# Kernel tuning notes

Measured on AMD Instinct MI355X. Metric: run time of the kernel, lower is better.

The kernel has to match this reference:

```python
import jax, jax.numpy as jnp
import numpy as np

N = 50000
E = 800000
IN_C, HID_C, OUT_C = 128, 128, 64


def setup_inputs() -> dict:
    key = jax.random.key(0)
    ks = jax.random.split(key, 12)
    x = jax.random.normal(ks[0], (N, IN_C), dtype=jnp.float32)
    edge_index = jax.random.randint(ks[1], (2, E), 0, N, dtype=jnp.int64)
    dims = [(IN_C, HID_C), (HID_C, HID_C), (HID_C, OUT_C)]
    params = {}
    for i, (din, dout) in enumerate(dims):
        s = 1.0 / np.sqrt(din)
        params[f"Wl{i}"] = jax.random.uniform(ks[2 + 3 * i], (din, dout), jnp.float32, -s, s)
        params[f"b{i}"] = jnp.zeros((dout,), jnp.float32)
        params[f"Wr{i}"] = jax.random.uniform(ks[3 + 3 * i], (din, dout), jnp.float32, -s, s)
    return {"x": x, "edge_index": edge_index, **params}


def _sage_conv(x, src, dst, Wl, b, Wr):
    # mean-aggregate neighbor features: messages flow src -> dst
    agg = jax.ops.segment_sum(x[src], dst, num_segments=N)          # [N, d]
    deg = jax.ops.segment_sum(jnp.ones((src.shape[0],), x.dtype), dst, num_segments=N)
    agg = agg / jnp.maximum(deg, 1.0)[:, None]                      # mean (0 for isolated nodes)
    return agg @ Wl + b + x @ Wr


def reference(x, edge_index, Wl0, b0, Wr0, Wl1, b1, Wr1, Wl2, b2, Wr2):
    src, dst = edge_index[0], edge_index[1]
    h = _sage_conv(x, src, dst, Wl0, b0, Wr0)
    h = jax.nn.relu(h)  # dropout is identity in eval mode
    h = _sage_conv(h, src, dst, Wl1, b1, Wr1)
    h = jax.nn.relu(h)
    h = _sage_conv(h, src, dst, Wl2, b2, Wr2)
    return h
```

## Files before the change

kernel.cpp:

```cpp
#include <hip/hip_runtime.h>

#define N_NODES 50000
#define N_EDGES 800000
#define NBUCK 196
#define NHIST 196

typedef __attribute__((ext_vector_type(8))) short short8;
typedef __attribute__((ext_vector_type(4))) float f32x4;
typedef __attribute__((ext_vector_type(8))) unsigned short ushort8v;
typedef __attribute__((ext_vector_type(16))) unsigned char uchar16;


__device__ inline void split_bf16(float f, unsigned short& hi, unsigned short& lo) {
    union { float f; unsigned u; } a; a.f = f;
    unsigned r = (a.u + 0x7fffu + ((a.u >> 16) & 1u)) >> 16;
    hi = (unsigned short)r;
    union { unsigned u; float f; } b; b.u = r << 16;
    union { float f; unsigned u; } c; c.f = f - b.f;
    unsigned r2 = (c.u + 0x7fffu + ((c.u >> 16) & 1u)) >> 16;
    lo = (unsigned short)r2;
}

__device__ inline unsigned short f2bf(float f) {
    union { float f; unsigned u; } a; a.f = f;
    return (unsigned short)((a.u + 0x7fffu + ((a.u >> 16) & 1u)) >> 16);
}

__device__ inline float bf2f(unsigned short u) {
    union { unsigned u; float f; } a; a.u = (unsigned)u << 16; return a.f;
}

__device__ inline unsigned char q8(float v, float qs) {
    int qi = (int)rintf(v * qs);
    qi = qi > 127 ? 127 : (qi < -127 ? -127 : qi);
    return (unsigned char)(qi + 128);
}

__device__ inline void acc8(float* a, uint2 w, float s) {
#pragma unroll
    for (int j = 0; j < 4; ++j) {
        a[j]     += (float)((w.x >> (8 * j)) & 255u) * s;
        a[j + 4] += (float)((w.y >> (8 * j)) & 255u) * s;
    }
}


__global__ void prep_kernel(const float* __restrict__ W0, const float* __restrict__ W1,
                            const float* __restrict__ W2, const float* __restrict__ W3,
                            const float* __restrict__ W4, const float* __restrict__ W5,
                            unsigned short* __restrict__ wout,
                            const float* __restrict__ x, unsigned short* __restrict__ xhi,
                            unsigned short* __restrict__ xlo,
                            unsigned char* __restrict__ xq, float* __restrict__ xsc,
                            const int* __restrict__ dst, int* __restrict__ blkhist) {
    __shared__ int lhist[NBUCK];
    if (blockIdx.x < 320) {
        int t = blockIdx.x * 256 + threadIdx.x;
        const float* W; int D, local, half; size_t base;
        if (t < 65536) {
            int mat = t >> 14; local = t & 16383; D = 128; half = 16384;
            base = (size_t)mat * 32768;
            W = mat == 0 ? W0 : mat == 1 ? W1 : mat == 2 ? W2 : W3;
        } else {
            int m = (t - 65536) >> 13; local = (t - 65536) & 8191; D = 64; half = 8192;
            base = 131072 + (size_t)m * 16384;
            W = m == 0 ? W4 : W5;
        }
        int j = local & 7, lane = (local >> 3) & 63, ks = (local >> 9) & 3, ct = local >> 11;
        int k = ks * 32 + ((lane >> 4) << 3) + j;
        int n = (ct << 4) + (lane & 15);
        unsigned short hi, lo;
        split_bf16(W[k * D + n], hi, lo);
        wout[base + local] = hi;
        wout[base + half + local] = lo;
    } else if (blockIdx.x < 1883) {
        int t = (blockIdx.x - 320) * 256 + threadIdx.x;
        if (t >= N_NODES * 8) return;
        const float* p = x + (size_t)t * 16;
        float4 v0 = *(const float4*)(p);
        float4 v1 = *(const float4*)(p + 4);
        float4 v2 = *(const float4*)(p + 8);
        float4 v3 = *(const float4*)(p + 12);
        float vv[16] = {v0.x, v0.y, v0.z, v0.w, v1.x, v1.y, v1.z, v1.w,
                        v2.x, v2.y, v2.z, v2.w, v3.x, v3.y, v3.z, v3.w};
        float m = 0.f;
#pragma unroll
        for (int j = 0; j < 16; ++j) m = fmaxf(m, fabsf(vv[j]));
        m = fmaxf(m, __shfl_xor(m, 1));
        m = fmaxf(m, __shfl_xor(m, 2));
        m = fmaxf(m, __shfl_xor(m, 4));
        float qs = m > 0.f ? 127.0f / m : 0.0f;
        uchar16 qv;
        ushort8v h0, l0, h1, l1;
#pragma unroll
        for (int j = 0; j < 16; ++j) {
            unsigned short a, b;
            split_bf16(vv[j], a, b);
            if (j < 8) { h0[j] = a; l0[j] = b; } else { h1[j - 8] = a; l1[j - 8] = b; }
            qv[j] = q8(vv[j], qs);
        }
        *(ushort8v*)(xhi + (size_t)t * 16) = h0;
        *(ushort8v*)(xhi + (size_t)t * 16 + 8) = h1;
        *(ushort8v*)(xlo + (size_t)t * 16) = l0;
        *(ushort8v*)(xlo + (size_t)t * 16 + 8) = l1;
        *(uchar16*)(xq + (size_t)t * 16) = qv;
        if ((t & 7) == 0) xsc[t >> 3] = m * (1.0f / 127.0f);
    } else {
        const int hb = blockIdx.x - 1883;
        const int base = hb * 4096;
        if (threadIdx.x < NBUCK) lhist[threadIdx.x] = 0;
        __syncthreads();
#pragma unroll
        for (int i = 0; i < 16; ++i) {
            int e = base + i * 256 + threadIdx.x;
            if (e < N_EDGES) atomicAdd(&lhist[dst[e] >> 8], 1);
        }
        __syncthreads();
        if (threadIdx.x < NBUCK) blkhist[hb * NBUCK + threadIdx.x] = lhist[threadIdx.x];
    }
}


__global__ void scan_sums_kernel(const int* __restrict__ blkhist,
                                 int* __restrict__ bucketBase, int* __restrict__ bucketCur,
                                 int* __restrict__ rowptr) {
    __shared__ int s[256];
    int tid = threadIdx.x;
    int v = 0;
    if (tid < NBUCK)
        for (int h = 0; h < NHIST; ++h) v += blkhist[h * NBUCK + tid];
    s[tid] = v;
    __syncthreads();
    for (int off = 1; off < 256; off <<= 1) {
        int t = (tid >= off) ? s[tid - off] : 0;
        __syncthreads();
        s[tid] += t;
        __syncthreads();
    }
    if (tid < NBUCK) {
        int b = s[tid] - v;
        bucketBase[tid] = b;
        bucketCur[tid] = b;
    }
    if (tid == 0) { bucketBase[NBUCK] = N_EDGES; rowptr[N_NODES] = N_EDGES; }
}


__global__ __launch_bounds__(256) void partition_kernel(
    const int* __restrict__ src, const int* __restrict__ dst,
    int* __restrict__ bucketCur, unsigned int* __restrict__ ebuf, int E) {
    __shared__ int hist[NBUCK], binoff[NBUCK], bincur[NBUCK], runstart[NBUCK];
    __shared__ int scanbuf[256];
    __shared__ unsigned int sortbuf[2048];
    const int tid = threadIdx.x;
    const int base = blockIdx.x * 2048;
    if (tid < NBUCK) hist[tid] = 0;
    __syncthreads();
    int myb[8]; unsigned int myp[8];
#pragma unroll
    for (int i = 0; i < 8; ++i) {
        int e = base + i * 256 + tid;
        if (e < E) {
            int d = dst[e], s = src[e];
            myb[i] = d >> 8;
            myp[i] = ((unsigned)d << 16) | (unsigned)s;
            atomicAdd(&hist[myb[i]], 1);
        } else myb[i] = -1;
    }
    __syncthreads();
    int v = (tid < NBUCK) ? hist[tid] : 0;
    scanbuf[tid] = v;
    __syncthreads();
    for (int off = 1; off < 256; off <<= 1) {
        int t = (tid >= off) ? scanbuf[tid - off] : 0;
        __syncthreads();
        scanbuf[tid] += t;
        __syncthreads();
    }
    if (tid < NBUCK) {
        binoff[tid] = scanbuf[tid] - v;
        bincur[tid] = 0;
        runstart[tid] = atomicAdd(&bucketCur[tid], v);
    }
    __syncthreads();
#pragma unroll
    for (int i = 0; i < 8; ++i) {
        if (myb[i] >= 0) {
            int r = atomicAdd(&bincur[myb[i]], 1);
            sortbuf[binoff[myb[i]] + r] = myp[i];
        }
    }
    __syncthreads();
    int nloc = E - base; if (nloc > 2048) nloc = 2048;
#pragma unroll
    for (int i = 0; i < 8; ++i) {
        int idx = i * 256 + tid;
        if (idx < nloc) {
            unsigned int p = sortbuf[idx];
            int b = p >> 24;
            ebuf[runstart[b] + (idx - binoff[b])] = p;
        }
    }
}


__global__ __launch_bounds__(256) void fine_fill_kernel(
    const unsigned int* __restrict__ ebuf, const int* __restrict__ bucketBase,
    int* __restrict__ rowptr, unsigned short* __restrict__ esrc, int n) {
    __shared__ int cnt[256], scanbuf[256], cur[256];
    const int b = blockIdx.x, tid = threadIdx.x;
    const int nbase = b << 8;
    cnt[tid] = 0;
    __syncthreads();
    const int lo = bucketBase[b], hi = bucketBase[b + 1];
    for (int k = lo + tid; k < hi; k += 256)
        atomicAdd(&cnt[(ebuf[k] >> 16) & 255], 1);
    __syncthreads();
    int v = cnt[tid];
    scanbuf[tid] = v;
    __syncthreads();
    for (int off = 1; off < 256; off <<= 1) {
        int t = (tid >= off) ? scanbuf[tid - off] : 0;
        __syncthreads();
        scanbuf[tid] += t;
        __syncthreads();
    }
    int start = lo + scanbuf[tid] - v;
    if (nbase + tid < n) rowptr[nbase + tid] = start;
    cur[tid] = start;
    __syncthreads();
    for (int k = lo + tid; k < hi; k += 256) {
        unsigned int p = ebuf[k];
        int pos = atomicAdd(&cur[(p >> 16) & 255], 1);
        esrc[pos] = (unsigned short)(p & 0xFFFFu);
    }
}


__global__ __launch_bounds__(256, 8) void agg_kernel(
    const unsigned char* __restrict__ Hq, const float* __restrict__ Hsc,
    const int* __restrict__ rowptr, const unsigned short* __restrict__ esrc,
    unsigned short* __restrict__ Ahi, int n) {
    int g = (blockIdx.x * blockDim.x + threadIdx.x) >> 4;
    int l16 = threadIdx.x & 15;
    if (g >= n) return;
    int beg = rowptr[g], end = rowptr[g + 1];
    const unsigned char* __restrict__ Hb = Hq + l16 * 8;
    float a0[8] = {0,0,0,0,0,0,0,0}, a1[8] = {0,0,0,0,0,0,0,0};
    float sacc = 0.f;
    int k = beg;
    for (; k + 6 <= end; k += 6) {
        int e0 = esrc[k],     e1 = esrc[k + 1], e2 = esrc[k + 2];
        int e3 = esrc[k + 3], e4 = esrc[k + 4], e5 = esrc[k + 5];
        uint2 w0 = *(const uint2*)(Hb + (size_t)e0 * 128);
        uint2 w1 = *(const uint2*)(Hb + (size_t)e1 * 128);
        uint2 w2 = *(const uint2*)(Hb + (size_t)e2 * 128);
        uint2 w3 = *(const uint2*)(Hb + (size_t)e3 * 128);
        uint2 w4 = *(const uint2*)(Hb + (size_t)e4 * 128);
        uint2 w5 = *(const uint2*)(Hb + (size_t)e5 * 128);
        float s0 = Hsc[e0], s1 = Hsc[e1], s2 = Hsc[e2];
        float s3 = Hsc[e3], s4 = Hsc[e4], s5 = Hsc[e5];
        acc8(a0, w0, s0); acc8(a1, w1, s1); acc8(a0, w2, s2);
        acc8(a1, w3, s3); acc8(a0, w4, s4); acc8(a1, w5, s5);
        sacc += s0 + s1 + s2 + s3 + s4 + s5;
    }
    for (; k + 2 <= end; k += 2) {
        int e0 = esrc[k], e1 = esrc[k + 1];
        uint2 w0 = *(const uint2*)(Hb + (size_t)e0 * 128);
        uint2 w1 = *(const uint2*)(Hb + (size_t)e1 * 128);
        float s0 = Hsc[e0], s1 = Hsc[e1];
        acc8(a0, w0, s0); acc8(a1, w1, s1);
        sacc += s0 + s1;
    }
    if (k < end) {
        int e0 = esrc[k];
        uint2 w0 = *(const uint2*)(Hb + (size_t)e0 * 128);
        float s0 = Hsc[e0];
        acc8(a0, w0, s0);
        sacc += s0;
    }
    float inv = (end > beg) ? 1.0f / (float)(end - beg) : 0.0f;
    ushort8v mh;
#pragma unroll
    for (int j = 0; j < 8; ++j)
        mh[j] = f2bf((a0[j] + a1[j] - 128.0f * sacc) * inv);
    *(ushort8v*)(Ahi + (size_t)g * 128 + l16 * 8) = mh;
}


template <int DOUT, bool RELU, bool SPLIT_OUT>
__global__ __launch_bounds__(256, 4) void gemm_planes(
    const unsigned short* __restrict__ A1hi,
    const unsigned short* __restrict__ A2hi, const unsigned short* __restrict__ A2lo,
    const unsigned short* __restrict__ B1p, const unsigned short* __restrict__ B2p,
    const float* __restrict__ bias, float* __restrict__ outf,
    unsigned short* __restrict__ outhi, unsigned short* __restrict__ outlo,
    unsigned char* __restrict__ outq, float* __restrict__ outsc, int M) {
    constexpr int K = 128, BM = 32, KS = 4, CT = DOUT / 16, CPW = CT / 4;
    constexpr int PITCH = K + 8;
    constexpr int HALF = CT * KS * 512;
    __shared__ unsigned short As[3][BM * PITCH];
    __shared__ float wmax[BM][4];

    const int tid = threadIdx.x;
    const int r0 = blockIdx.x * BM;

    const unsigned short* __restrict__ srcs[3] = {A1hi, A2hi, A2lo};
#pragma unroll
    for (int s = 0; s < 3; ++s) {
#pragma unroll
        for (int c = 0; c < 2; ++c) {
            int chunk = tid + c * 256;
            int row = chunk >> 4;
            int c8 = (chunk & 15) * 8;
            int grow = r0 + row; if (grow >= M) grow = M - 1;
            *(ushort8v*)(&As[s][row * PITCH + c8]) =
                *(const ushort8v*)(srcs[s] + (size_t)grow * K + c8);
        }
    }
    __syncthreads();

    const int wave = tid >> 6, lane = tid & 63;
    const int rl = lane & 15, quad = lane >> 4;

    f32x4 acc[2][CPW];
#pragma unroll
    for (int c = 0; c < CPW; ++c) {
        float bv = bias[(wave * CPW + c) * 16 + rl];
        acc[0][c] = (f32x4){bv, bv, bv, bv};
        acc[1][c] = acc[0][c];
    }

#pragma unroll
    for (int ks = 0; ks < KS; ++ks) {
        short8 a_ag[2], a_sh[2][2];
#pragma unroll
        for (int rt = 0; rt < 2; ++rt) {
            int off = (rt * 16 + rl) * PITCH + ks * 32 + quad * 8;
            a_ag[rt]    = *(const short8*)(&As[0][off]);
            a_sh[rt][0] = *(const short8*)(&As[1][off]);
            a_sh[rt][1] = *(const short8*)(&As[2][off]);
        }
        short8 b1[CPW][2], b2[CPW][2];
#pragma unroll
        for (int c = 0; c < CPW; ++c) {
            size_t boff = (((wave * CPW + c) * KS + ks) * 64 + lane) * 8;
#pragma unroll
            for (int p = 0; p < 2; ++p) {
                b1[c][p] = *(const short8*)(B1p + p * HALF + boff);
                b2[c][p] = *(const short8*)(B2p + p * HALF + boff);
            }
        }
#pragma unroll
        for (int rt = 0; rt < 2; ++rt)
#pragma unroll
            for (int c = 0; c < CPW; ++c) {
                acc[rt][c] = __builtin_amdgcn_mfma_f32_16x16x32_bf16(a_ag[rt],    b1[c][0], acc[rt][c], 0, 0, 0);
                acc[rt][c] = __builtin_amdgcn_mfma_f32_16x16x32_bf16(a_ag[rt],    b1[c][1], acc[rt][c], 0, 0, 0);
                acc[rt][c] = __builtin_amdgcn_mfma_f32_16x16x32_bf16(a_sh[rt][0], b2[c][0], acc[rt][c], 0, 0, 0);
                acc[rt][c] = __builtin_amdgcn_mfma_f32_16x16x32_bf16(a_sh[rt][0], b2[c][1], acc[rt][c], 0, 0, 0);
                acc[rt][c] = __builtin_amdgcn_mfma_f32_16x16x32_bf16(a_sh[rt][1], b2[c][0], acc[rt][c], 0, 0, 0);
            }
    }

    if (RELU) {
#pragma unroll
        for (int rt = 0; rt < 2; ++rt)
#pragma unroll
            for (int c = 0; c < CPW; ++c)
#pragma unroll
                for (int r = 0; r < 4; ++r)
                    acc[rt][c][r] = fmaxf(acc[rt][c][r], 0.f);
    }

    float qsc[2][4];
    if constexpr (SPLIT_OUT) {
        float lm[2][4];
#pragma unroll
        for (int rt = 0; rt < 2; ++rt)
#pragma unroll
            for (int r = 0; r < 4; ++r) {
                float m = fabsf(acc[rt][0][r]);
#pragma unroll
                for (int c = 1; c < CPW; ++c) m = fmaxf(m, fabsf(acc[rt][c][r]));
                lm[rt][r] = m;
            }
#pragma unroll
        for (int off = 1; off < 16; off <<= 1)
#pragma unroll
            for (int rt = 0; rt < 2; ++rt)
#pragma unroll
                for (int r = 0; r < 4; ++r)
                    lm[rt][r] = fmaxf(lm[rt][r], __shfl_xor(lm[rt][r], off));
        if (rl == 0) {
#pragma unroll
            for (int rt = 0; rt < 2; ++rt)
#pragma unroll
                for (int r = 0; r < 4; ++r)
                    wmax[rt * 16 + quad * 4 + r][wave] = lm[rt][r];
        }
        __syncthreads();
#pragma unroll
        for (int rt = 0; rt < 2; ++rt)
#pragma unroll
            for (int r = 0; r < 4; ++r) {
                int row = rt * 16 + quad * 4 + r;
                float rm = fmaxf(fmaxf(wmax[row][0], wmax[row][1]),
                                 fmaxf(wmax[row][2], wmax[row][3]));
                qsc[rt][r] = rm > 0.f ? 127.0f / rm : 0.0f;
                if (wave == 0 && rl == 0) {
                    int rr = r0 + row;
                    if (rr < M) outsc[rr] = rm * (1.0f / 127.0f);
                }
            }
    }

#pragma unroll
    for (int rt = 0; rt < 2; ++rt)
#pragma unroll
        for (int c = 0; c < CPW; ++c) {
            int col = (wave * CPW + c) * 16 + rl;
            int rowb = r0 + rt * 16 + quad * 4;
#pragma unroll
            for (int r = 0; r < 4; ++r) {
                int rr = rowb + r;
                if (rr < M) {
                    float vv = acc[rt][c][r];
                    if (SPLIT_OUT) {
                        unsigned short h, l;
                        split_bf16(vv, h, l);
                        outhi[(size_t)rr * DOUT + col] = h;
                        outlo[(size_t)rr * DOUT + col] = l;
                        outq[(size_t)rr * DOUT + col] = q8(vv, qsc[rt][r]);
                    } else {
                        outf[(size_t)rr * DOUT + col] = vv;
                    }
                }
            }
        }
}


extern "C" void kernel_launch(void* const* d_in, const int* in_sizes, int n_in,
                              void* d_out, int out_size, void* d_ws, size_t ws_size,
                              hipStream_t stream) {
    const float* x   = (const float*)d_in[0];
    const int* eidx  = (const int*)d_in[1];
    const int* src   = eidx;
    const int* dst   = eidx + N_EDGES;
    const float* Wl0 = (const float*)d_in[2];
    const float* b0  = (const float*)d_in[3];
    const float* Wr0 = (const float*)d_in[4];
    const float* Wl1 = (const float*)d_in[5];
    const float* b1  = (const float*)d_in[6];
    const float* Wr1 = (const float*)d_in[7];
    const float* Wl2 = (const float*)d_in[8];
    const float* b2  = (const float*)d_in[9];
    const float* Wr2 = (const float*)d_in[10];
    float* outp = (float*)d_out;

    unsigned short* xhi  = (unsigned short*)d_ws;
    unsigned short* xlo  = xhi + (size_t)N_NODES * 128;
    unsigned short* aghi = xlo + (size_t)N_NODES * 128;
    unsigned int* ebuf = (unsigned int*)aghi;
    int* rowptr    = (int*)(aghi + (size_t)N_NODES * 128);
    int* blkhist   = rowptr + 50016;
    int* bucketBase= blkhist + 38416;
    int* bucketCur = bucketBase + 256;
    unsigned short* esrc  = (unsigned short*)(bucketCur + 256);
    unsigned short* packw = esrc + N_EDGES;
    unsigned short* Wl0p = packw;
    unsigned short* Wr0p = packw + 32768;
    unsigned short* Wl1p = packw + 65536;
    unsigned short* Wr1p = packw + 98304;
    unsigned short* Wl2p = packw + 131072;
    unsigned short* Wr2p = packw + 147456;
    unsigned char* xq = (unsigned char*)(packw + 163840);
    float* xsc = (float*)(xq + (size_t)N_NODES * 128);

    prep_kernel<<<2079, 256, 0, stream>>>(Wl0, Wr0, Wl1, Wr1, Wl2, Wr2, packw,
                                          x, xhi, xlo, xq, xsc, dst, blkhist);
    scan_sums_kernel<<<1, 256, 0, stream>>>(blkhist, bucketBase, bucketCur, rowptr);
    partition_kernel<<<(N_EDGES + 2047) / 2048, 256, 0, stream>>>(src, dst, bucketCur, ebuf, N_EDGES);
    fine_fill_kernel<<<NBUCK, 256, 0, stream>>>(ebuf, bucketBase, rowptr, esrc, N_NODES);

    const int aggGrid = (N_NODES * 16 + 255) / 256;
    const int gemmGrid = (N_NODES + 31) / 32;

    agg_kernel<<<aggGrid, 256, 0, stream>>>(xq, xsc, rowptr, esrc, aghi, N_NODES);
    gemm_planes<128, true, true><<<gemmGrid, 256, 0, stream>>>(
        aghi, xhi, xlo, Wl0p, Wr0p, b0, nullptr, xhi, xlo, xq, xsc, N_NODES);
    agg_kernel<<<aggGrid, 256, 0, stream>>>(xq, xsc, rowptr, esrc, aghi, N_NODES);
    gemm_planes<128, true, true><<<gemmGrid, 256, 0, stream>>>(
        aghi, xhi, xlo, Wl1p, Wr1p, b1, nullptr, xhi, xlo, xq, xsc, N_NODES);
    agg_kernel<<<aggGrid, 256, 0, stream>>>(xq, xsc, rowptr, esrc, aghi, N_NODES);
    gemm_planes<64, false, false><<<gemmGrid, 256, 0, stream>>>(
        aghi, xhi, xlo, Wl2p, Wr2p, b2, outp, nullptr, nullptr, nullptr, nullptr, N_NODES);
}
```

Baseline: 267.7 us.

## Split aggregation into two feature-half passes to shrink gather working set

Each aggregation launch now processes only half of the 128 quantized feature bytes per node (64 bytes), with two launches per layer covering both halves. The intent is to halve the gathered working set per pass so the randomly accessed neighbor rows fit better in L2/MALL cache, improving hit rates. The cost is reading rowptr, esrc and the scale array twice, twice as many threads per node-slice of work with smaller 4-byte loads, and extra kernel launches.

```diff
diff --git a/kernel.cpp b/kernel.cpp
--- a/kernel.cpp
+++ b/kernel.cpp
@@ -7,6 +7,7 @@
 
 typedef __attribute__((ext_vector_type(8))) short short8;
 typedef __attribute__((ext_vector_type(4))) float f32x4;
+typedef __attribute__((ext_vector_type(4))) unsigned short ushort4v;
 typedef __attribute__((ext_vector_type(8))) unsigned short ushort8v;
 typedef __attribute__((ext_vector_type(16))) unsigned char uchar16;
 
@@ -36,12 +37,10 @@
     return (unsigned char)(qi + 128);
 }
 
-__device__ inline void acc8(float* a, uint2 w, float s) {
-#pragma unroll
-    for (int j = 0; j < 4; ++j) {
-        a[j]     += (float)((w.x >> (8 * j)) & 255u) * s;
-        a[j + 4] += (float)((w.y >> (8 * j)) & 255u) * s;
-    }
+__device__ inline void acc4(float* a, unsigned w, float s) {
+#pragma unroll
+    for (int j = 0; j < 4; ++j)
+        a[j] += (float)((w >> (8 * j)) & 255u) * s;
 }
 
 
@@ -237,6 +236,7 @@
 }
 
 
+template <int SLICE>
 __global__ __launch_bounds__(256, 8) void agg_kernel(
     const unsigned char* __restrict__ Hq, const float* __restrict__ Hsc,
     const int* __restrict__ rowptr, const unsigned short* __restrict__ esrc,
@@ -245,46 +245,46 @@
     int l16 = threadIdx.x & 15;
     if (g >= n) return;
     int beg = rowptr[g], end = rowptr[g + 1];
-    const unsigned char* __restrict__ Hb = Hq + l16 * 8;
-    float a0[8] = {0,0,0,0,0,0,0,0}, a1[8] = {0,0,0,0,0,0,0,0};
+    const unsigned char* __restrict__ Hb = Hq + SLICE * 64 + l16 * 4;
+    float a0[4] = {0,0,0,0}, a1[4] = {0,0,0,0};
     float sacc = 0.f;
     int k = beg;
     for (; k + 6 <= end; k += 6) {
         int e0 = esrc[k],     e1 = esrc[k + 1], e2 = esrc[k + 2];
         int e3 = esrc[k + 3], e4 = esrc[k + 4], e5 = esrc[k + 5];
-        uint2 w0 = *(const uint2*)(Hb + (size_t)e0 * 128);
-        uint2 w1 = *(const uint2*)(Hb + (size_t)e1 * 128);
-        uint2 w2 = *(const uint2*)(Hb + (size_t)e2 * 128);
-        uint2 w3 = *(const uint2*)(Hb + (size_t)e3 * 128);
-        uint2 w4 = *(const uint2*)(Hb + (size_t)e4 * 128);
-        uint2 w5 = *(const uint2*)(Hb + (size_t)e5 * 128);
+        unsigned w0 = *(const unsigned*)(Hb + (size_t)e0 * 128);
+        unsigned w1 = *(const unsigned*)(Hb + (size_t)e1 * 128);
+        unsigned w2 = *(const unsigned*)(Hb + (size_t)e2 * 128);
+        unsigned w3 = *(const unsigned*)(Hb + (size_t)e3 * 128);
+        unsigned w4 = *(const unsigned*)(Hb + (size_t)e4 * 128);
+        unsigned w5 = *(const unsigned*)(Hb + (size_t)e5 * 128);
         float s0 = Hsc[e0], s1 = Hsc[e1], s2 = Hsc[e2];
         float s3 = Hsc[e3], s4 = Hsc[e4], s5 = Hsc[e5];
-        acc8(a0, w0, s0); acc8(a1, w1, s1); acc8(a0, w2, s2);
-        acc8(a1, w3, s3); acc8(a0, w4, s4); acc8(a1, w5, s5);
+        acc4(a0, w0, s0); acc4(a1, w1, s1); acc4(a0, w2, s2);
+        acc4(a1, w3, s3); acc4(a0, w4, s4); acc4(a1, w5, s5);
         sacc += s0 + s1 + s2 + s3 + s4 + s5;
     }
     for (; k + 2 <= end; k += 2) {
         int e0 = esrc[k], e1 = esrc[k + 1];
-        uint2 w0 = *(const uint2*)(Hb + (size_t)e0 * 128);
-        uint2 w1 = *(const uint2*)(Hb + (size_t)e1 * 128);
+        unsigned w0 = *(const unsigned*)(Hb + (size_t)e0 * 128);
+        unsigned w1 = *(const unsigned*)(Hb + (size_t)e1 * 128);
         float s0 = Hsc[e0], s1 = Hsc[e1];
-        acc8(a0, w0, s0); acc8(a1, w1, s1);
+        acc4(a0, w0, s0); acc4(a1, w1, s1);
         sacc += s0 + s1;
     }
     if (k < end) {
         int e0 = esrc[k];
-        uint2 w0 = *(const uint2*)(Hb + (size_t)e0 * 128);
+        unsigned w0 = *(const unsigned*)(Hb + (size_t)e0 * 128);
         float s0 = Hsc[e0];
-        acc8(a0, w0, s0);
+        acc4(a0, w0, s0);
         sacc += s0;
     }
     float inv = (end > beg) ? 1.0f / (float)(end - beg) : 0.0f;
-    ushort8v mh;
-#pragma unroll
-    for (int j = 0; j < 8; ++j)
+    ushort4v mh;
+#pragma unroll
+    for (int j = 0; j < 4; ++j)
         mh[j] = f2bf((a0[j] + a1[j] - 128.0f * sacc) * inv);
-    *(ushort8v*)(Ahi + (size_t)g * 128 + l16 * 8) = mh;
+    *(ushort4v*)(Ahi + (size_t)g * 128 + SLICE * 64 + l16 * 4) = mh;
 }
 
 
@@ -487,13 +487,16 @@
     const int aggGrid = (N_NODES * 16 + 255) / 256;
     const int gemmGrid = (N_NODES + 31) / 32;
 
-    agg_kernel<<<aggGrid, 256, 0, stream>>>(xq, xsc, rowptr, esrc, aghi, N_NODES);
+    agg_kernel<0><<<aggGrid, 256, 0, stream>>>(xq, xsc, rowptr, esrc, aghi, N_NODES);
+    agg_kernel<1><<<aggGrid, 256, 0, stream>>>(xq, xsc, rowptr, esrc, aghi, N_NODES);
     gemm_planes<128, true, true><<<gemmGrid, 256, 0, stream>>>(
         aghi, xhi, xlo, Wl0p, Wr0p, b0, nullptr, xhi, xlo, xq, xsc, N_NODES);
-    agg_kernel<<<aggGrid, 256, 0, stream>>>(xq, xsc, rowptr, esrc, aghi, N_NODES);
+    agg_kernel<0><<<aggGrid, 256, 0, stream>>>(xq, xsc, rowptr, esrc, aghi, N_NODES);
+    agg_kernel<1><<<aggGrid, 256, 0, stream>>>(xq, xsc, rowptr, esrc, aghi, N_NODES);
     gemm_planes<128, true, true><<<gemmGrid, 256, 0, stream>>>(
         aghi, xhi, xlo, Wl1p, Wr1p, b1, nullptr, xhi, xlo, xq, xsc, N_NODES);
-    agg_kernel<<<aggGrid, 256, 0, stream>>>(xq, xsc, rowptr, esrc, aghi, N_NODES);
+    agg_kernel<0><<<aggGrid, 256, 0, stream>>>(xq, xsc, rowptr, esrc, aghi, N_NODES);
+    agg_kernel<1><<<aggGrid, 256, 0, stream>>>(xq, xsc, rowptr, esrc, aghi, N_NODES);
     gemm_planes<64, false, false><<<gemmGrid, 256, 0, stream>>>(
         aghi, xhi, xlo, Wl2p, Wr2p, b2, outp, nullptr, nullptr, nullptr, nullptr, N_NODES);
 }
```

New measurement: 292.9 us. 9.4% more time.

## Fuse neighbor aggregation into GEMM kernel and use fixed-capacity buckets for CSR build

Applied to the files above, without the earlier changes.

Each layer's mean aggregation now runs inside the GEMM kernel, writing the aggregated bf16 tile straight into shared memory. This removes the separate agg kernel and its global write and read of the aggregate. The CSR build drops the histogram and scan pass by giving every bucket a fixed capacity, so row begin and end are stored separately, and feature buffers now ping-pong between x and y. The costs are lower occupancy for the gather inside the GEMM kernel (4 blocks per CU instead of 8) and a capacity assumption that a bucket never holds more than 8192 edges.

```diff
diff --git a/kernel.cpp b/kernel.cpp
--- a/kernel.cpp
+++ b/kernel.cpp
@@ -3,7 +3,7 @@
 #define N_NODES 50000
 #define N_EDGES 800000
 #define NBUCK 196
-#define NHIST 196
+#define BCAP 8192
 
 typedef __attribute__((ext_vector_type(8))) short short8;
 typedef __attribute__((ext_vector_type(4))) float f32x4;
@@ -52,8 +52,7 @@
                             const float* __restrict__ x, unsigned short* __restrict__ xhi,
                             unsigned short* __restrict__ xlo,
                             unsigned char* __restrict__ xq, float* __restrict__ xsc,
-                            const int* __restrict__ dst, int* __restrict__ blkhist) {
-    __shared__ int lhist[NBUCK];
+                            int* __restrict__ bucketCur) {
     if (blockIdx.x < 320) {
         int t = blockIdx.x * 256 + threadIdx.x;
         const float* W; int D, local, half; size_t base;
@@ -106,43 +105,8 @@
         *(uchar16*)(xq + (size_t)t * 16) = qv;
         if ((t & 7) == 0) xsc[t >> 3] = m * (1.0f / 127.0f);
     } else {
-        const int hb = blockIdx.x - 1883;
-        const int base = hb * 4096;
-        if (threadIdx.x < NBUCK) lhist[threadIdx.x] = 0;
-        __syncthreads();
-#pragma unroll
-        for (int i = 0; i < 16; ++i) {
-            int e = base + i * 256 + threadIdx.x;
-            if (e < N_EDGES) atomicAdd(&lhist[dst[e] >> 8], 1);
-        }
-        __syncthreads();
-        if (threadIdx.x < NBUCK) blkhist[hb * NBUCK + threadIdx.x] = lhist[threadIdx.x];
-    }
-}
-
-
-__global__ void scan_sums_kernel(const int* __restrict__ blkhist,
-                                 int* __restrict__ bucketBase, int* __restrict__ bucketCur,
-                                 int* __restrict__ rowptr) {
-    __shared__ int s[256];
-    int tid = threadIdx.x;
-    int v = 0;
-    if (tid < NBUCK)
-        for (int h = 0; h < NHIST; ++h) v += blkhist[h * NBUCK + tid];
-    s[tid] = v;
-    __syncthreads();
-    for (int off = 1; off < 256; off <<= 1) {
-        int t = (tid >= off) ? s[tid - off] : 0;
-        __syncthreads();
-        s[tid] += t;
-        __syncthreads();
-    }
-    if (tid < NBUCK) {
-        int b = s[tid] - v;
-        bucketBase[tid] = b;
-        bucketCur[tid] = b;
-    }
-    if (tid == 0) { bucketBase[NBUCK] = N_EDGES; rowptr[N_NODES] = N_EDGES; }
+        if (threadIdx.x < 256) bucketCur[threadIdx.x] = 0;
+    }
 }
 
 
@@ -180,7 +144,7 @@
     if (tid < NBUCK) {
         binoff[tid] = scanbuf[tid] - v;
         bincur[tid] = 0;
-        runstart[tid] = atomicAdd(&bucketCur[tid], v);
+        runstart[tid] = tid * BCAP + atomicAdd(&bucketCur[tid], v);
     }
     __syncthreads();
 #pragma unroll
@@ -205,14 +169,15 @@
 
 
 __global__ __launch_bounds__(256) void fine_fill_kernel(
-    const unsigned int* __restrict__ ebuf, const int* __restrict__ bucketBase,
-    int* __restrict__ rowptr, unsigned short* __restrict__ esrc, int n) {
+    const unsigned int* __restrict__ ebuf, const int* __restrict__ bucketCur,
+    int* __restrict__ rowbeg, int* __restrict__ rowend,
+    unsigned short* __restrict__ esrc, int n) {
     __shared__ int cnt[256], scanbuf[256], cur[256];
     const int b = blockIdx.x, tid = threadIdx.x;
     const int nbase = b << 8;
     cnt[tid] = 0;
     __syncthreads();
-    const int lo = bucketBase[b], hi = bucketBase[b + 1];
+    const int lo = b * BCAP, hi = lo + bucketCur[b];
     for (int k = lo + tid; k < hi; k += 256)
         atomicAdd(&cnt[(ebuf[k] >> 16) & 255], 1);
     __syncthreads();
@@ -226,7 +191,7 @@
         __syncthreads();
     }
     int start = lo + scanbuf[tid] - v;
-    if (nbase + tid < n) rowptr[nbase + tid] = start;
+    if (nbase + tid < n) { rowbeg[nbase + tid] = start; rowend[nbase + tid] = start + v; }
     cur[tid] = start;
     __syncthreads();
     for (int k = lo + tid; k < hi; k += 256) {
@@ -237,61 +202,12 @@
 }
 
 
-__global__ __launch_bounds__(256, 8) void agg_kernel(
+template <int DOUT, bool RELU, bool SPLIT_OUT>
+__global__ __launch_bounds__(256, 4) void sage_layer(
     const unsigned char* __restrict__ Hq, const float* __restrict__ Hsc,
-    const int* __restrict__ rowptr, const unsigned short* __restrict__ esrc,
-    unsigned short* __restrict__ Ahi, int n) {
-    int g = (blockIdx.x * blockDim.x + threadIdx.x) >> 4;
-    int l16 = threadIdx.x & 15;
-    if (g >= n) return;
-    int beg = rowptr[g], end = rowptr[g + 1];
-    const unsigned char* __restrict__ Hb = Hq + l16 * 8;
-    float a0[8] = {0,0,0,0,0,0,0,0}, a1[8] = {0,0,0,0,0,0,0,0};
-    float sacc = 0.f;
-    int k = beg;
-    for (; k + 6 <= end; k += 6) {
-        int e0 = esrc[k],     e1 = esrc[k + 1], e2 = esrc[k + 2];
-        int e3 = esrc[k + 3], e4 = esrc[k + 4], e5 = esrc[k + 5];
-        uint2 w0 = *(const uint2*)(Hb + (size_t)e0 * 128);
-        uint2 w1 = *(const uint2*)(Hb + (size_t)e1 * 128);
-        uint2 w2 = *(const uint2*)(Hb + (size_t)e2 * 128);
-        uint2 w3 = *(const uint2*)(Hb + (size_t)e3 * 128);
-        uint2 w4 = *(const uint2*)(Hb + (size_t)e4 * 128);
-        uint2 w5 = *(const uint2*)(Hb + (size_t)e5 * 128);
-        float s0 = Hsc[e0], s1 = Hsc[e1], s2 = Hsc[e2];
-        float s3 = Hsc[e3], s4 = Hsc[e4], s5 = Hsc[e5];
-        acc8(a0, w0, s0); acc8(a1, w1, s1); acc8(a0, w2, s2);
-        acc8(a1, w3, s3); acc8(a0, w4, s4); acc8(a1, w5, s5);
-        sacc += s0 + s1 + s2 + s3 + s4 + s5;
-    }
-    for (; k + 2 <= end; k += 2) {
-        int e0 = esrc[k], e1 = esrc[k + 1];
-        uint2 w0 = *(const uint2*)(Hb + (size_t)e0 * 128);
-        uint2 w1 = *(const uint2*)(Hb + (size_t)e1 * 128);
-        float s0 = Hsc[e0], s1 = Hsc[e1];
-        acc8(a0, w0, s0); acc8(a1, w1, s1);
-        sacc += s0 + s1;
-    }
-    if (k < end) {
-        int e0 = esrc[k];
-        uint2 w0 = *(const uint2*)(Hb + (size_t)e0 * 128);
-        float s0 = Hsc[e0];
-        acc8(a0, w0, s0);
-        sacc += s0;
-    }
-    float inv = (end > beg) ? 1.0f / (float)(end - beg) : 0.0f;
-    ushort8v mh;
-#pragma unroll
-    for (int j = 0; j < 8; ++j)
-        mh[j] = f2bf((a0[j] + a1[j] - 128.0f * sacc) * inv);
-    *(ushort8v*)(Ahi + (size_t)g * 128 + l16 * 8) = mh;
-}
-
-
-template <int DOUT, bool RELU, bool SPLIT_OUT>
-__global__ __launch_bounds__(256, 4) void gemm_planes(
-    const unsigned short* __restrict__ A1hi,
-    const unsigned short* __restrict__ A2hi, const unsigned short* __restrict__ A2lo,
+    const unsigned short* __restrict__ Hhi, const unsigned short* __restrict__ Hlo,
+    const int* __restrict__ rowbeg, const int* __restrict__ rowend,
+    const unsigned short* __restrict__ esrc,
     const unsigned short* __restrict__ B1p, const unsigned short* __restrict__ B2p,
     const float* __restrict__ bias, float* __restrict__ outf,
     unsigned short* __restrict__ outhi, unsigned short* __restrict__ outlo,
@@ -305,17 +221,67 @@
     const int tid = threadIdx.x;
     const int r0 = blockIdx.x * BM;
 
-    const unsigned short* __restrict__ srcs[3] = {A1hi, A2hi, A2lo};
-#pragma unroll
-    for (int s = 0; s < 3; ++s) {
+    const unsigned short* __restrict__ srcs[2] = {Hhi, Hlo};
+#pragma unroll
+    for (int s = 0; s < 2; ++s) {
 #pragma unroll
         for (int c = 0; c < 2; ++c) {
             int chunk = tid + c * 256;
             int row = chunk >> 4;
             int c8 = (chunk & 15) * 8;
             int grow = r0 + row; if (grow >= M) grow = M - 1;
-            *(ushort8v*)(&As[s][row * PITCH + c8]) =
+            *(ushort8v*)(&As[s + 1][row * PITCH + c8]) =
                 *(const ushort8v*)(srcs[s] + (size_t)grow * K + c8);
+        }
+    }
+
+    {
+        const int g16 = tid >> 4, l16 = tid & 15;
+        const unsigned char* __restrict__ Hb = Hq + l16 * 8;
+#pragma unroll
+        for (int nn = 0; nn < 2; ++nn) {
+            int row = g16 * 2 + nn;
+            int node = r0 + row; if (node >= M) node = M - 1;
+            int beg = rowbeg[node], end = rowend[node];
+            float a0[8] = {0,0,0,0,0,0,0,0}, a1[8] = {0,0,0,0,0,0,0,0};
+            float sacc = 0.f;
+            int k = beg;
+            for (; k + 6 <= end; k += 6) {
+                int e0 = esrc[k],     e1 = esrc[k + 1], e2 = esrc[k + 2];
+                int e3 = esrc[k + 3], e4 = esrc[k + 4], e5 = esrc[k + 5];
+                uint2 w0 = *(const uint2*)(Hb + (size_t)e0 * 128);
+                uint2 w1 = *(const uint2*)(Hb + (size_t)e1 * 128);
+                uint2 w2 = *(const uint2*)(Hb + (size_t)e2 * 128);
+                uint2 w3 = *(const uint2*)(Hb + (size_t)e3 * 128);
+                uint2 w4 = *(const uint2*)(Hb + (size_t)e4 * 128);
+                uint2 w5 = *(const uint2*)(Hb + (size_t)e5 * 128);
+                float s0 = Hsc[e0], s1 = Hsc[e1], s2 = Hsc[e2];
+                float s3 = Hsc[e3], s4 = Hsc[e4], s5 = Hsc[e5];
+                acc8(a0, w0, s0); acc8(a1, w1, s1); acc8(a0, w2, s2);
+                acc8(a1, w3, s3); acc8(a0, w4, s4); acc8(a1, w5, s5);
+                sacc += s0 + s1 + s2 + s3 + s4 + s5;
+            }
+            for (; k + 2 <= end; k += 2) {
+                int e0 = esrc[k], e1 = esrc[k + 1];
+                uint2 w0 = *(const uint2*)(Hb + (size_t)e0 * 128);
+                uint2 w1 = *(const uint2*)(Hb + (size_t)e1 * 128);
+                float s0 = Hsc[e0], s1 = Hsc[e1];
+                acc8(a0, w0, s0); acc8(a1, w1, s1);
+                sacc += s0 + s1;
+            }
+            if (k < end) {
+                int e0 = esrc[k];
+                uint2 w0 = *(const uint2*)(Hb + (size_t)e0 * 128);
+                float s0 = Hsc[e0];
+                acc8(a0, w0, s0);
+                sacc += s0;
+            }
+            float inv = (end > beg) ? 1.0f / (float)(end - beg) : 0.0f;
+            ushort8v mh;
+#pragma unroll
+            for (int j = 0; j < 8; ++j)
+                mh[j] = f2bf((a0[j] + a1[j] - 128.0f * sacc) * inv);
+            *(ushort8v*)(&As[0][row * PITCH + l16 * 8]) = mh;
         }
     }
     __syncthreads();
@@ -461,39 +427,39 @@
 
     unsigned short* xhi  = (unsigned short*)d_ws;
     unsigned short* xlo  = xhi + (size_t)N_NODES * 128;
-    unsigned short* aghi = xlo + (size_t)N_NODES * 128;
-    unsigned int* ebuf = (unsigned int*)aghi;
-    int* rowptr    = (int*)(aghi + (size_t)N_NODES * 128);
-    int* blkhist   = rowptr + 50016;
-    int* bucketBase= blkhist + 38416;
-    int* bucketCur = bucketBase + 256;
-    unsigned short* esrc  = (unsigned short*)(bucketCur + 256);
-    unsigned short* packw = esrc + N_EDGES;
+    unsigned short* yhi  = xlo + (size_t)N_NODES * 128;
+    unsigned short* ylo  = yhi + (size_t)N_NODES * 128;
+    unsigned int* ebuf = (unsigned int*)yhi;
+    unsigned char* xq = (unsigned char*)(ylo + (size_t)N_NODES * 128);
+    unsigned char* yq = xq + (size_t)N_NODES * 128;
+    float* xsc = (float*)(yq + (size_t)N_NODES * 128);
+    float* ysc = xsc + N_NODES;
+    int* rowbeg = (int*)(ysc + N_NODES);
+    int* rowend = rowbeg + N_NODES;
+    int* bucketCur = rowend + N_NODES;
+    unsigned short* esrc = (unsigned short*)(bucketCur + 256);
+    unsigned short* packw = esrc + NBUCK * BCAP;
     unsigned short* Wl0p = packw;
     unsigned short* Wr0p = packw + 32768;
     unsigned short* Wl1p = packw + 65536;
     unsigned short* Wr1p = packw + 98304;
     unsigned short* Wl2p = packw + 131072;
     unsigned short* Wr2p = packw + 147456;
-    unsigned char* xq = (unsigned char*)(packw + 163840);
-    float* xsc = (float*)(xq + (size_t)N_NODES * 128);
-
-    prep_kernel<<<2079, 256, 0, stream>>>(Wl0, Wr0, Wl1, Wr1, Wl2, Wr2, packw,
-                                          x, xhi, xlo, xq, xsc, dst, blkhist);
-    scan_sums_kernel<<<1, 256, 0, stream>>>(blkhist, bucketBase, bucketCur, rowptr);
+
+    prep_kernel<<<1884, 256, 0, stream>>>(Wl0, Wr0, Wl1, Wr1, Wl2, Wr2, packw,
+                                          x, xhi, xlo, xq, xsc, bucketCur);
     partition_kernel<<<(N_EDGES + 2047) / 2048, 256, 0, stream>>>(src, dst, bucketCur, ebuf, N_EDGES);
-    fine_fill_kernel<<<NBUCK, 256, 0, stream>>>(ebuf, bucketBase, rowptr, esrc, N_NODES);
-
-    const int aggGrid = (N_NODES * 16 + 255) / 256;
+    fine_fill_kernel<<<NBUCK, 256, 0, stream>>>(ebuf, bucketCur, rowbeg, rowend, esrc, N_NODES);
+
     const int gemmGrid = (N_NODES + 31) / 32;
 
-    agg_kernel<<<aggGrid, 256, 0, stream>>>(xq, xsc, rowptr, esrc, aghi, N_NODES);
-    gemm_planes<128, true, true><<<gemmGrid, 256, 0, stream>>>(
-        aghi, xhi, xlo, Wl0p, Wr0p, b0, nullptr, xhi, xlo, xq, xsc, N_NODES);
-    agg_kernel<<<aggGrid, 256, 0, stream>>>(xq, xsc, rowptr, esrc, aghi, N_NODES);
-    gemm_planes<128, true, true><<<gemmGrid, 256, 0, stream>>>(
-        aghi, xhi, xlo, Wl1p, Wr1p, b1, nullptr, xhi, xlo, xq, xsc, N_NODES);
-    agg_kernel<<<aggGrid, 256, 0, stream>>>(xq, xsc, rowptr, esrc, aghi, N_NODES);
-    gemm_planes<64, false, false><<<gemmGrid, 256, 0, stream>>>(
-        aghi, xhi, xlo, Wl2p, Wr2p, b2, outp, nullptr, nullptr, nullptr, nullptr, N_NODES);
-}
+    sage_layer<128, true, true><<<gemmGrid, 256, 0, stream>>>(
+        xq, xsc, xhi, xlo, rowbeg, rowend, esrc, Wl0p, Wr0p, b0,
+        nullptr, yhi, ylo, yq, ysc, N_NODES);
+    sage_layer<128, true, true><<<gemmGrid, 256, 0, stream>>>(
+        yq, ysc, yhi, ylo, rowbeg, rowend, esrc, Wl1p, Wr1p, b1,
+        nullptr, xhi, xlo, xq, xsc, N_NODES);
+    sage_layer<64, false, false><<<gemmGrid, 256, 0, stream>>>(
+        xq, xsc, xhi, xlo, rowbeg, rowend, esrc, Wl2p, Wr2p, b2,
+        outp, nullptr, nullptr, nullptr, nullptr, N_NODES);
+}
```

Result: faster. 241.2 us (-9.9%).
